# Performance work log

Hardware: AMD Instinct MI355X
Metric: run time of the kernel (lower is better)

The kernel has to match this reference:

```python
import jax, jax.numpy as jnp
import numpy as np

H_INP = 128
H_DIM = 128
NUM_WORD = 15000
NUM_TOPIC = 50
B = 32                 # number of graphs in the batch
DOCS_PER_GRAPH = 512
N_DOC = B * DOCS_PER_GRAPH        # 16384
N_WORD_NODES = 100_000
N_TOPIC_NODES = B * NUM_TOPIC     # 1600
E_WD = 1_000_000
E_TD = 200_000


def graph_conv(x_src, src, dst, n_src, n_dst, W, b):
    """DGL GraphConv with norm='both', sum aggregation: out = D_dst^{-1/2} A D_src^{-1/2} X W + b."""
    ones = jnp.ones(src.shape[0], x_src.dtype)
    outdeg = jnp.clip(jax.ops.segment_sum(ones, src, num_segments=n_src), 1.0)
    indeg = jnp.clip(jax.ops.segment_sum(ones, dst, num_segments=n_dst), 1.0)
    x = x_src * jax.lax.rsqrt(outdeg)[:, None]
    agg = jax.ops.segment_sum(x[src], dst, num_segments=n_dst)   # [n_dst, h_in]
    return (agg @ W) * jax.lax.rsqrt(indeg)[:, None] + b


def setup_inputs() -> dict:
    key = jax.random.key(0)
    ks = jax.random.split(key, 16)
    inp = {
        "word_ids": jax.random.randint(ks[0], (N_WORD_NODES,), 0, NUM_WORD),
        "topic_ids": jax.random.randint(ks[1], (N_TOPIC_NODES,), 0, NUM_TOPIC),
        "wd_src": jax.random.randint(ks[2], (E_WD,), 0, N_WORD_NODES),
        "wd_dst": jax.random.randint(ks[3], (E_WD,), 0, N_DOC),
        "td_src": jax.random.randint(ks[4], (E_TD,), 0, N_TOPIC_NODES),
        "td_dst": jax.random.randint(ks[5], (E_TD,), 0, N_DOC),
        "y_data": jax.random.uniform(ks[6], (B,), jnp.float32),
        "word_embeds": jax.random.normal(ks[7], (NUM_WORD, H_INP), jnp.float32) * 0.02,
        "topic_embeds": jax.random.normal(ks[8], (NUM_TOPIC, H_DIM), jnp.float32) * 0.02,
        "W_wd": jax.random.normal(ks[9], (H_INP, H_DIM), jnp.float32) * 0.05,
        "b_wd": jnp.zeros((H_DIM,), jnp.float32),
        "W_td": jax.random.normal(ks[10], (H_DIM, H_DIM), jnp.float32) * 0.05,
        "b_td": jnp.zeros((H_DIM,), jnp.float32),
        "W_out": jax.random.normal(ks[11], (H_DIM, 1), jnp.float32) * 0.05,
        "b_out": jnp.zeros((1,), jnp.float32),
    }
    return inp


def reference(word_ids, topic_ids, wd_src, wd_dst, td_src, td_dst, y_data,
              word_embeds, topic_embeds, W_wd, b_wd, W_td, b_td, W_out, b_out):
    # embedding gathers for word / topic node features (doc input features are zeros)
    word_emb = word_embeds[word_ids]          # [N_word_nodes, h_inp]
    topic_emb = topic_embeds[topic_ids]       # [N_topic_nodes, h_dim]
    # HeteroGraphConv with aggregate='sum'; only 'doc' output is consumed,
    # which receives messages from relations 'wd' (word->doc) and 'td' (topic->doc).
    doc_wd = graph_conv(word_emb, wd_src, wd_dst, N_WORD_NODES, N_DOC, W_wd, b_wd)
    doc_td = graph_conv(topic_emb, td_src, td_dst, N_TOPIC_NODES, N_DOC, W_td, b_td)
    doc_emb = doc_wd + doc_td                 # [N_DOC, h_dim]
    # split per graph, pad, mean over padded axis (equal doc counts => plain reshape-mean)
    doc_pool = doc_emb.reshape(B, DOCS_PER_GRAPH, H_DIM).mean(axis=1)  # [B, h_dim]
    logits = doc_pool @ W_out + b_out         # [B, 1]
    x = logits.reshape(-1)
    # binary_cross_entropy_with_logits (mean reduction), numerically stable
    loss = jnp.mean(jnp.maximum(x, 0.0) - x * y_data + jnp.log1p(jnp.exp(-jnp.abs(x))))
    y_pred = jax.nn.sigmoid(logits)
    return loss, y_pred
```

## Files before the change

### kernel.cpp

```cpp
#include <hip/hip_runtime.h>
#include <hip/hip_bf16.h>

#define NWN    100000
#define NTN    1600
#define NDOC   16384
#define EWD    1000000
#define ETD    200000
#define NWORD  15000
#define NTOPIC 50
#define HD     128
#define NB     32
#define NSW    64
#define NSD    64
#define NST    32
#define WRDW   25000
#define NBLK_E 256
#define BDIM_E 640
#define STRIDE_E (NBLK_E * BDIM_E)
#define NU4    300000
#define NWAVE_E (BDIM_E / 64)

#define O_SLABW 0
#define O_SLABD 1600000
#define O_SLABT 2648576
#define O_DOCS  2699776
#define O_UNW   2716160
#define O_UNT   2816160
#define O_V     2817760
#define O_UW    2818016
#define O_UT    2833016
#define O_ACC   2833080
#define O_CNT   2833112

__global__ void __launch_bounds__(1024) a_histv(const int* __restrict__ wd_src,
                                                const int* __restrict__ wd_dst,
                                                const int* __restrict__ td_src,
                                                const int* __restrict__ td_dst,
                                                const float* __restrict__ Wwd,
                                                const float* __restrict__ Wtd,
                                                const float* __restrict__ Wout,
                                                unsigned* __restrict__ ws) {
    __shared__ unsigned h[WRDW];
    int tid = threadIdx.x;
    int b   = blockIdx.x;
    if (b < NSW) {
        for (int k = tid; k < WRDW; k += 1024) h[k] = 0u;
        __syncthreads();
        const int4* p = (const int4*)wd_src;
        for (int i = b * 1024 + tid; i < EWD / 4; i += NSW * 1024) {
            int4 s = p[i];
            atomicAdd(&h[((unsigned)s.x) >> 2], 1u << (8 * (s.x & 3)));
            atomicAdd(&h[((unsigned)s.y) >> 2], 1u << (8 * (s.y & 3)));
            atomicAdd(&h[((unsigned)s.z) >> 2], 1u << (8 * (s.z & 3)));
            atomicAdd(&h[((unsigned)s.w) >> 2], 1u << (8 * (s.w & 3)));
        }
        __syncthreads();
        unsigned* slab = ws + O_SLABW + b * WRDW;
        for (int k = tid; k < WRDW; k += 1024) slab[k] = h[k];
    } else if (b < NSW + NSD) {
        int sb = b - NSW;
        for (int k = tid; k < NDOC; k += 1024) h[k] = 0u;
        __syncthreads();
        const int4* p = (const int4*)wd_dst;
        for (int i = sb * 1024 + tid; i < EWD / 4; i += NSD * 1024) {
            int4 d = p[i];
            atomicAdd(&h[d.x], 1u); atomicAdd(&h[d.y], 1u);
            atomicAdd(&h[d.z], 1u); atomicAdd(&h[d.w], 1u);
        }
        const int4* q = (const int4*)td_dst;
        for (int i = sb * 1024 + tid; i < ETD / 4; i += NSD * 1024) {
            int4 d = q[i];
            atomicAdd(&h[d.x], 65536u); atomicAdd(&h[d.y], 65536u);
            atomicAdd(&h[d.z], 65536u); atomicAdd(&h[d.w], 65536u);
        }
        __syncthreads();
        unsigned* slab = ws + O_SLABD + sb * NDOC;
        for (int k = tid; k < NDOC; k += 1024) slab[k] = h[k];
    } else if (b < NSW + NSD + NST) {
        int sb = b - NSW - NSD;
        for (int k = tid; k < NTN; k += 1024) h[k] = 0u;
        __syncthreads();
        const int4* p = (const int4*)td_src;
        for (int i = sb * 1024 + tid; i < ETD / 4; i += NST * 1024) {
            int4 s = p[i];
            atomicAdd(&h[s.x], 1u); atomicAdd(&h[s.y], 1u);
            atomicAdd(&h[s.z], 1u); atomicAdd(&h[s.w], 1u);
        }
        __syncthreads();
        unsigned* slab = ws + O_SLABT + sb * NTN;
        for (int k = tid; k < NTN; k += 1024) slab[k] = h[k];
    } else {
        if (tid < HD) {
            float* hw = (float*)h;
            hw[tid] = Wout[tid];
            __syncthreads();
            float s1 = 0.f, s2 = 0.f;
            for (int j = 0; j < HD; ++j) {
                s1 += Wwd[tid * HD + j] * hw[j];
                s2 += Wtd[tid * HD + j] * hw[j];
            }
            float* v = (float*)(ws + O_V);
            v[tid]      = s1;
            v[tid + HD] = s2;
            if (tid < NB) ((float*)(ws + O_ACC))[tid] = 0.f;
            if (tid == NB) ws[O_CNT] = 0u;
        } else {
            __syncthreads();
        }
    }
}

__global__ void f_u(const float* __restrict__ wemb, const float* __restrict__ temb,
                    unsigned* __restrict__ ws) {
    const float* v = (const float*)(ws + O_V);
    int wave = threadIdx.x >> 6;
    int lane = threadIdx.x & 63;
    int row  = blockIdx.x * (blockDim.x >> 6) + wave;
    const float* src; const float* vv; float* dst; int r;
    if (row < NWORD) {
        src = wemb; vv = v; dst = (float*)(ws + O_UW); r = row;
    } else if (row < NWORD + NTOPIC) {
        src = temb; vv = v + HD; dst = (float*)(ws + O_UT); r = row - NWORD;
    } else return;
    float s = src[r * HD + lane]      * vv[lane]
            + src[r * HD + lane + 64] * vv[lane + 64];
    #pragma unroll
    for (int off = 32; off; off >>= 1) s += __shfl_down(s, off);
    if (lane == 0) dst[r] = s;
}

__global__ void f_un(const int* __restrict__ wids, const int* __restrict__ tids,
                     unsigned* __restrict__ ws) {
    const unsigned* slabW = ws + O_SLABW;
    const unsigned* slabD = ws + O_SLABD;
    const unsigned* slabT = ws + O_SLABT;
    unsigned* docs = ws + O_DOCS;
    const float* u_wd = (const float*)(ws + O_UW);
    const float* u_td = (const float*)(ws + O_UT);
    float* un_w = (float*)(ws + O_UNW);
    float* un_t = (float*)(ws + O_UNT);
    int t = blockIdx.x * blockDim.x + threadIdx.x;
    if (t < NWN) {
        int w = t >> 2, sh = 8 * (t & 3);
        unsigned d = 0u;
        #pragma unroll
        for (int j = 0; j < NSW; ++j) d += (slabW[j * WRDW + w] >> sh) & 0xFFu;
        un_w[t] = u_wd[wids[t]] * rsqrtf((float)(d > 1u ? d : 1u));
    } else if (t < NWN + NDOC) {
        int k = t - NWN;
        unsigned s = 0u;
        #pragma unroll
        for (int j = 0; j < NSD; ++j) s += slabD[j * NDOC + k];
        docs[k] = s;
    } else if (t < NWN + NDOC + NTN) {
        int k = t - NWN - NDOC;
        unsigned d = 0u;
        #pragma unroll
        for (int j = 0; j < NST; ++j) d += slabT[j * NTN + k];
        un_t[k] = u_td[tids[k]] * rsqrtf((float)(d > 1u ? d : 1u));
    }
}

__global__ void __launch_bounds__(BDIM_E) d_edges_fin(const int* __restrict__ wd_src,
                                                      const int* __restrict__ wd_dst,
                                                      const int* __restrict__ td_src,
                                                      const int* __restrict__ td_dst,
                                                      const float* __restrict__ y_data,
                                                      const float* __restrict__ b_wd,
                                                      const float* __restrict__ b_td,
                                                      const float* __restrict__ Wout,
                                                      const float* __restrict__ b_out,
                                                      unsigned* __restrict__ ws,
                                                      float* __restrict__ out) {
    const unsigned* docs = ws + O_DOCS;
    const float* un_w = (const float*)(ws + O_UNW);
    const float* un_t = (const float*)(ws + O_UNT);
    float* acc = (float*)(ws + O_ACC);
    __shared__ float lacc[NWAVE_E][NB];
    __shared__ unsigned lastflag;
    int tid = threadIdx.x;
    int wv  = tid >> 6;
    if (tid < NWAVE_E * NB) ((float*)lacc)[tid] = 0.f;
    __syncthreads();
    float* wacc = lacc[wv];

    int4 sv[2], dv[2];
    int kind[2];
    int gid = blockIdx.x * BDIM_E + tid;
    #pragma unroll
    for (int k = 0; k < 2; ++k) {
        int u = gid + k * STRIDE_E;
        if (u < EWD / 4) {
            sv[k] = ((const int4*)wd_src)[u];
            dv[k] = ((const int4*)wd_dst)[u];
            kind[k] = 0;
        } else if (u < NU4) {
            int e = u - EWD / 4;
            sv[k] = ((const int4*)td_src)[e];
            dv[k] = ((const int4*)td_dst)[e];
            kind[k] = 1;
        } else {
            kind[k] = 2;
        }
    }
    #pragma unroll
    for (int k = 0; k < 2; ++k) {
        int4 s = sv[k], d = dv[k];
        unsigned b;
        if (kind[k] == 0) {
            b = docs[d.x] & 0xFFFFu;
            atomicAdd(&wacc[d.x >> 9], un_w[s.x] * rsqrtf((float)(b > 1u ? b : 1u)));
            b = docs[d.y] & 0xFFFFu;
            atomicAdd(&wacc[d.y >> 9], un_w[s.y] * rsqrtf((float)(b > 1u ? b : 1u)));
            b = docs[d.z] & 0xFFFFu;
            atomicAdd(&wacc[d.z >> 9], un_w[s.z] * rsqrtf((float)(b > 1u ? b : 1u)));
            b = docs[d.w] & 0xFFFFu;
            atomicAdd(&wacc[d.w >> 9], un_w[s.w] * rsqrtf((float)(b > 1u ? b : 1u)));
        } else if (kind[k] == 1) {
            b = docs[d.x] >> 16;
            atomicAdd(&wacc[d.x >> 9], un_t[s.x] * rsqrtf((float)(b > 1u ? b : 1u)));
            b = docs[d.y] >> 16;
            atomicAdd(&wacc[d.y >> 9], un_t[s.y] * rsqrtf((float)(b > 1u ? b : 1u)));
            b = docs[d.z] >> 16;
            atomicAdd(&wacc[d.z >> 9], un_t[s.z] * rsqrtf((float)(b > 1u ? b : 1u)));
            b = docs[d.w] >> 16;
            atomicAdd(&wacc[d.w >> 9], un_t[s.w] * rsqrtf((float)(b > 1u ? b : 1u)));
        }
    }
    __syncthreads();
    if (tid < NB) {
        float s = 0.f;
        #pragma unroll
        for (int j = 0; j < NWAVE_E; ++j) s += lacc[j][tid];
        atomicAdd(&acc[tid], s);
    }
    if (tid == 0) {
        __threadfence();
        unsigned prev = atomicAdd(&ws[O_CNT], 1u);
        lastflag = (prev == (unsigned)gridDim.x - 1u) ? 1u : 0u;
    }
    __syncthreads();
    if (lastflag && tid < 64) {
        float p = (b_wd[tid] + b_td[tid]) * Wout[tid]
                + (b_wd[tid + 64] + b_td[tid + 64]) * Wout[tid + 64];
        #pragma unroll
        for (int off = 32; off; off >>= 1) p += __shfl_down(p, off);
        float c0 = __shfl(p, 0) + b_out[0];
        float l = 0.f;
        if (tid < NB) {
            float a = atomicAdd(&acc[tid], 0.0f);
            float x = a * (1.0f / 512.0f) + c0;
            float y = y_data[tid];
            l = fmaxf(x, 0.f) - x * y + log1pf(expf(-fabsf(x)));
            out[1 + tid] = 1.0f / (1.0f + expf(-x));
        }
        #pragma unroll
        for (int off = 16; off; off >>= 1) l += __shfl_down(l, off);
        if (tid == 0) out[0] = l * (1.0f / (float)NB);
    }
}

extern "C" void kernel_launch(void* const* d_in, const int* in_sizes, int n_in,
                              void* d_out, int out_size, void* d_ws, size_t ws_size,
                              hipStream_t stream) {
    const int* word_ids  = (const int*)d_in[0];
    const int* topic_ids = (const int*)d_in[1];
    const int* wd_src    = (const int*)d_in[2];
    const int* wd_dst    = (const int*)d_in[3];
    const int* td_src    = (const int*)d_in[4];
    const int* td_dst    = (const int*)d_in[5];
    const float* y_data  = (const float*)d_in[6];
    const float* wemb    = (const float*)d_in[7];
    const float* temb    = (const float*)d_in[8];
    const float* Wwd     = (const float*)d_in[9];
    const float* bwd     = (const float*)d_in[10];
    const float* Wtd     = (const float*)d_in[11];
    const float* btd     = (const float*)d_in[12];
    const float* Wout    = (const float*)d_in[13];
    const float* bout    = (const float*)d_in[14];
    float* out = (float*)d_out;
    unsigned* ws = (unsigned*)d_ws;

    a_histv<<<NSW + NSD + NST + 1, 1024, 0, stream>>>(
        wd_src, wd_dst, td_src, td_dst, Wwd, Wtd, Wout, ws);
    f_u<<<(NWORD + NTOPIC + 3) / 4, 256, 0, stream>>>(wemb, temb, ws);
    f_un<<<(NWN + NDOC + NTN + 255) / 256, 256, 0, stream>>>(word_ids, topic_ids, ws);
    d_edges_fin<<<NBLK_E, BDIM_E, 0, stream>>>(wd_src, wd_dst, td_src, td_dst,
                                               y_data, bwd, btd, Wout, bout, ws, out);
}
```

Baseline: 39.57 us.

## Fuse embedding projection into histogram kernel and stage doc degrees in LDS

Drops the separate f_u launch by adding 64 extra blocks to the histogram kernel. Each of these blocks recomputes the projected vectors W·Wout locally and then projects its share of embedding rows, so launches go from four to three. The edge kernel now copies the packed doc-degree array (64 KB) into shared memory before the edge loop, so lookups are LDS reads rather than scattered global loads. The cost is redundant W·Wout work in every projection block and a 64 KB LDS footprint per edge block, which may limit occupancy and adds a copy phase.

```diff
diff --git a/kernel.cpp b/kernel.cpp
--- a/kernel.cpp
+++ b/kernel.cpp
@@ -13,6 +13,7 @@
 #define NSW    64
 #define NSD    64
 #define NST    32
+#define NSU    64
 #define WRDW   25000
 #define NBLK_E 256
 #define BDIM_E 640
@@ -26,20 +27,21 @@
 #define O_DOCS  2699776
 #define O_UNW   2716160
 #define O_UNT   2816160
-#define O_V     2817760
-#define O_UW    2818016
-#define O_UT    2833016
-#define O_ACC   2833080
-#define O_CNT   2833112
-
-__global__ void __launch_bounds__(1024) a_histv(const int* __restrict__ wd_src,
-                                                const int* __restrict__ wd_dst,
-                                                const int* __restrict__ td_src,
-                                                const int* __restrict__ td_dst,
-                                                const float* __restrict__ Wwd,
-                                                const float* __restrict__ Wtd,
-                                                const float* __restrict__ Wout,
-                                                unsigned* __restrict__ ws) {
+#define O_UW    2816768
+#define O_UT    2831768
+#define O_ACC   2831832
+#define O_CNT   2831864
+
+__global__ void __launch_bounds__(1024) a_histuv(const int* __restrict__ wd_src,
+                                                 const int* __restrict__ wd_dst,
+                                                 const int* __restrict__ td_src,
+                                                 const int* __restrict__ td_dst,
+                                                 const float* __restrict__ wemb,
+                                                 const float* __restrict__ temb,
+                                                 const float* __restrict__ Wwd,
+                                                 const float* __restrict__ Wtd,
+                                                 const float* __restrict__ Wout,
+                                                 unsigned* __restrict__ ws) {
     __shared__ unsigned h[WRDW];
     int tid = threadIdx.x;
     int b   = blockIdx.x;
@@ -89,44 +91,40 @@
         __syncthreads();
         unsigned* slab = ws + O_SLABT + sb * NTN;
         for (int k = tid; k < NTN; k += 1024) slab[k] = h[k];
+    } else if (b < NSW + NSD + NST + NSU) {
+        int ub = b - NSW - NSD - NST;
+        float* hw = (float*)h;
+        if (tid < HD) hw[tid] = Wout[tid];
+        __syncthreads();
+        if (tid < HD) {
+            float s1 = 0.f;
+            for (int j = 0; j < HD; ++j) s1 += Wwd[tid * HD + j] * hw[j];
+            hw[HD + tid] = s1;
+        } else if (tid < 2 * HD) {
+            int t2 = tid - HD;
+            float s2 = 0.f;
+            for (int j = 0; j < HD; ++j) s2 += Wtd[t2 * HD + j] * hw[j];
+            hw[2 * HD + t2] = s2;
+        }
+        __syncthreads();
+        int wave = tid >> 6;
+        int lane = tid & 63;
+        float* u_wd = (float*)(ws + O_UW);
+        float* u_td = (float*)(ws + O_UT);
+        for (int row = ub * 16 + wave; row < NWORD + NTOPIC; row += NSU * 16) {
+            const float* src; const float* vv; float* dst; int r;
+            if (row < NWORD) { src = wemb; vv = hw + HD;     dst = u_wd; r = row; }
+            else             { src = temb; vv = hw + 2 * HD; dst = u_td; r = row - NWORD; }
+            float s = src[r * HD + lane]      * vv[lane]
+                    + src[r * HD + lane + 64] * vv[lane + 64];
+            #pragma unroll
+            for (int off = 32; off; off >>= 1) s += __shfl_down(s, off);
+            if (lane == 0) dst[r] = s;
+        }
     } else {
-        if (tid < HD) {
-            float* hw = (float*)h;
-            hw[tid] = Wout[tid];
-            __syncthreads();
-            float s1 = 0.f, s2 = 0.f;
-            for (int j = 0; j < HD; ++j) {
-                s1 += Wwd[tid * HD + j] * hw[j];
-                s2 += Wtd[tid * HD + j] * hw[j];
-            }
-            float* v = (float*)(ws + O_V);
-            v[tid]      = s1;
-            v[tid + HD] = s2;
-            if (tid < NB) ((float*)(ws + O_ACC))[tid] = 0.f;
-            if (tid == NB) ws[O_CNT] = 0u;
-        } else {
-            __syncthreads();
-        }
-    }
-}
-
-__global__ void f_u(const float* __restrict__ wemb, const float* __restrict__ temb,
-                    unsigned* __restrict__ ws) {
-    const float* v = (const float*)(ws + O_V);
-    int wave = threadIdx.x >> 6;
-    int lane = threadIdx.x & 63;
-    int row  = blockIdx.x * (blockDim.x >> 6) + wave;
-    const float* src; const float* vv; float* dst; int r;
-    if (row < NWORD) {
-        src = wemb; vv = v; dst = (float*)(ws + O_UW); r = row;
-    } else if (row < NWORD + NTOPIC) {
-        src = temb; vv = v + HD; dst = (float*)(ws + O_UT); r = row - NWORD;
-    } else return;
-    float s = src[r * HD + lane]      * vv[lane]
-            + src[r * HD + lane + 64] * vv[lane + 64];
-    #pragma unroll
-    for (int off = 32; off; off >>= 1) s += __shfl_down(s, off);
-    if (lane == 0) dst[r] = s;
+        if (tid < NB) ((float*)(ws + O_ACC))[tid] = 0.f;
+        if (tid == NB) ws[O_CNT] = 0u;
+    }
 }
 
 __global__ void f_un(const int* __restrict__ wids, const int* __restrict__ tids,
@@ -172,17 +170,14 @@
                                                       const float* __restrict__ b_out,
                                                       unsigned* __restrict__ ws,
                                                       float* __restrict__ out) {
-    const unsigned* docs = ws + O_DOCS;
     const float* un_w = (const float*)(ws + O_UNW);
     const float* un_t = (const float*)(ws + O_UNT);
     float* acc = (float*)(ws + O_ACC);
+    __shared__ unsigned sdocs[NDOC];
     __shared__ float lacc[NWAVE_E][NB];
     __shared__ unsigned lastflag;
     int tid = threadIdx.x;
     int wv  = tid >> 6;
-    if (tid < NWAVE_E * NB) ((float*)lacc)[tid] = 0.f;
-    __syncthreads();
-    float* wacc = lacc[wv];
 
     int4 sv[2], dv[2];
     int kind[2];
@@ -203,27 +198,36 @@
             kind[k] = 2;
         }
     }
+    {
+        const uint4* dsrc = (const uint4*)(ws + O_DOCS);
+        uint4* ddst = (uint4*)sdocs;
+        for (int k = tid; k < NDOC / 4; k += BDIM_E) ddst[k] = dsrc[k];
+        if (tid < NWAVE_E * NB) ((float*)lacc)[tid] = 0.f;
+    }
+    __syncthreads();
+    float* wacc = lacc[wv];
+
     #pragma unroll
     for (int k = 0; k < 2; ++k) {
         int4 s = sv[k], d = dv[k];
         unsigned b;
         if (kind[k] == 0) {
-            b = docs[d.x] & 0xFFFFu;
+            b = sdocs[d.x] & 0xFFFFu;
             atomicAdd(&wacc[d.x >> 9], un_w[s.x] * rsqrtf((float)(b > 1u ? b : 1u)));
-            b = docs[d.y] & 0xFFFFu;
+            b = sdocs[d.y] & 0xFFFFu;
             atomicAdd(&wacc[d.y >> 9], un_w[s.y] * rsqrtf((float)(b > 1u ? b : 1u)));
-            b = docs[d.z] & 0xFFFFu;
+            b = sdocs[d.z] & 0xFFFFu;
             atomicAdd(&wacc[d.z >> 9], un_w[s.z] * rsqrtf((float)(b > 1u ? b : 1u)));
-            b = docs[d.w] & 0xFFFFu;
+            b = sdocs[d.w] & 0xFFFFu;
             atomicAdd(&wacc[d.w >> 9], un_w[s.w] * rsqrtf((float)(b > 1u ? b : 1u)));
         } else if (kind[k] == 1) {
-            b = docs[d.x] >> 16;
+            b = sdocs[d.x] >> 16;
             atomicAdd(&wacc[d.x >> 9], un_t[s.x] * rsqrtf((float)(b > 1u ? b : 1u)));
-            b = docs[d.y] >> 16;
+            b = sdocs[d.y] >> 16;
             atomicAdd(&wacc[d.y >> 9], un_t[s.y] * rsqrtf((float)(b > 1u ? b : 1u)));
-            b = docs[d.z] >> 16;
+            b = sdocs[d.z] >> 16;
             atomicAdd(&wacc[d.z >> 9], un_t[s.z] * rsqrtf((float)(b > 1u ? b : 1u)));
-            b = docs[d.w] >> 16;
+            b = sdocs[d.w] >> 16;
             atomicAdd(&wacc[d.w >> 9], un_t[s.w] * rsqrtf((float)(b > 1u ? b : 1u)));
         }
     }
@@ -281,9 +285,8 @@
     float* out = (float*)d_out;
     unsigned* ws = (unsigned*)d_ws;
 
-    a_histv<<<NSW + NSD + NST + 1, 1024, 0, stream>>>(
-        wd_src, wd_dst, td_src, td_dst, Wwd, Wtd, Wout, ws);
-    f_u<<<(NWORD + NTOPIC + 3) / 4, 256, 0, stream>>>(wemb, temb, ws);
+    a_histuv<<<NSW + NSD + NST + NSU + 1, 1024, 0, stream>>>(
+        wd_src, wd_dst, td_src, td_dst, wemb, temb, Wwd, Wtd, Wout, ws);
     f_un<<<(NWN + NDOC + NTN + 255) / 256, 256, 0, stream>>>(word_ids, topic_ids, ws);
     d_edges_fin<<<NBLK_E, BDIM_E, 0, stream>>>(wd_src, wd_dst, td_src, td_dst,
                                                y_data, bwd, btd, Wout, bout, ws, out);
```

New measurement: 44.33 us. +12.0%, slower.
